# Kernel tuning notes

Hardware: AMD Instinct MI355X
Metric: run time of the kernel (lower is better)

## Reference

```python
import jax, jax.numpy as jnp
import numpy as np

N_T, N_C, N_M = 300000, 100000, 20000
D_IN, D, D_OUT = 390, 128, 64
H_PRE, H_POST = 256, 64


def _nrm(k, shape, scale=0.02):
    return jax.random.normal(k, shape, dtype=jnp.float32) * scale


def setup_inputs() -> dict:
    key = jax.random.key(0)
    ks = jax.random.split(key, 24)
    inp = {
        'input_features': jax.random.normal(ks[0], (N_T, D_IN), jnp.float32),
        'card_of_target': jax.random.randint(ks[1], (N_T,), 0, N_C, jnp.int32),
        'merchant_of_target': jax.random.randint(ks[2], (N_T,), 0, N_M, jnp.int32),
        # HeteroEmbedding tables for src types feeding 'target'
        'card_emb': _nrm(ks[3], (N_C, D)),
        'merch_emb': _nrm(ks[4], (N_M, D)),
        # target_preprocessing FFBlock (390 -> 256 -> 128, n_layers=2)
        'pre_Wi': _nrm(ks[5], (D_IN, H_PRE)), 'pre_bi': jnp.zeros((H_PRE,), jnp.float32),
        'pre_Wh': _nrm(ks[6], (H_PRE, H_PRE)), 'pre_bh': jnp.zeros((H_PRE,), jnp.float32),
        'pre_Wo': _nrm(ks[7], (H_PRE, D)), 'pre_bo': jnp.zeros((D,), jnp.float32),
        # conv1 / conv2: one GraphConv per etype; order:
        # 0=card->target, 1=merchant->target, 2=target->card, 3=target->merchant
        'conv1_W': _nrm(ks[8], (4, D, D)), 'conv1_b': jnp.zeros((4, D), jnp.float32),
        'conv2_W': _nrm(ks[9], (4, D, D)), 'conv2_b': jnp.zeros((4, D), jnp.float32),
        # conv3: dst=='target' -> D_OUT; dst!='target' -> 1
        'conv3_Wt': _nrm(ks[10], (2, D, D_OUT)), 'conv3_bt': jnp.zeros((2, D_OUT), jnp.float32),
        'conv3_Wo': _nrm(ks[11], (2, D, 1)), 'conv3_bo': jnp.zeros((2, 1), jnp.float32),
        # target_postprocessing FFBlock (64 -> 64 -> 1, n_layers=2)
        'post_Wi': _nrm(ks[12], (D_OUT, H_POST)), 'post_bi': jnp.zeros((H_POST,), jnp.float32),
        'post_Wh': _nrm(ks[13], (H_POST, H_POST)), 'post_bh': jnp.zeros((H_POST,), jnp.float32),
        'post_Wo': _nrm(ks[14], (H_POST, 1)), 'post_bo': jnp.zeros((1,), jnp.float32),
    }
    return inp


def _ff(x, Wi, bi, Wh, bh, Wo, bo, n_layers=2):
    h = jax.nn.relu(x @ Wi + bi)
    for _ in range(1, n_layers):
        h = jax.nn.relu(h @ Wh + bh)
    return h @ Wo + bo


def _deg(ids, n):
    # degree per node over edge endpoint list, clamped to >= 1 (DGL GraphConv)
    return jnp.maximum(jnp.zeros((n,), jnp.float32).at[ids].add(1.0), 1.0)


def _gconv(x_src, src, dst, n_dst, W, b, d_src, d_dst):
    # DGL GraphConv, norm='both': scale src by out_deg^-1/2, matmul,
    # sum messages onto dst, scale by in_deg^-1/2, add bias.
    h = (x_src * jax.lax.rsqrt(d_src)[:, None]) @ W          # [n_src, out]
    agg = jax.ops.segment_sum(h[src], dst, num_segments=n_dst)
    return agg * jax.lax.rsqrt(d_dst)[:, None] + b


def reference(input_features, card_of_target, merchant_of_target,
              card_emb, merch_emb,
              pre_Wi, pre_bi, pre_Wh, pre_bh, pre_Wo, pre_bo,
              conv1_W, conv1_b, conv2_W, conv2_b,
              conv3_Wt, conv3_bt, conv3_Wo, conv3_bo,
              post_Wi, post_bi, post_Wh, post_bh, post_Wo, post_bo):
    n_t, n_c, n_m = input_features.shape[0], card_emb.shape[0], merch_emb.shape[0]
    t_ids = jnp.arange(n_t, dtype=jnp.int32)
    d_c = _deg(card_of_target, n_c)      # card degree (in/out symmetric here)
    d_m = _deg(merchant_of_target, n_m)  # merchant degree
    d_t = _deg(t_ids, n_t)               # target degree (=1 per etype)

    tf = _ff(input_features, pre_Wi, pre_bi, pre_Wh, pre_bh, pre_Wo, pre_bo)

    # conv1 (HeteroGraphConv, aggregate='sum') + relu
    h1_t = (_gconv(card_emb, card_of_target, t_ids, n_t, conv1_W[0], conv1_b[0], d_c, d_t)
            + _gconv(merch_emb, merchant_of_target, t_ids, n_t, conv1_W[1], conv1_b[1], d_m, d_t))
    h1_c = _gconv(tf, t_ids, card_of_target, n_c, conv1_W[2], conv1_b[2], d_t, d_c)
    h1_m = _gconv(tf, t_ids, merchant_of_target, n_m, conv1_W[3], conv1_b[3], d_t, d_m)
    h1_t, h1_c, h1_m = jax.nn.relu(h1_t), jax.nn.relu(h1_c), jax.nn.relu(h1_m)

    # conv2 applied (conv_layers - 2) = 1 time
    h2_t, h2_c, h2_m = h1_t, h1_c, h1_m
    for _ in range(2, 3):
        n_t2 = (_gconv(h2_c, card_of_target, t_ids, n_t, conv2_W[0], conv2_b[0], d_c, d_t)
                + _gconv(h2_m, merchant_of_target, t_ids, n_t, conv2_W[1], conv2_b[1], d_m, d_t))
        n_c2 = _gconv(h2_t, t_ids, card_of_target, n_c, conv2_W[2], conv2_b[2], d_t, d_c)
        n_m2 = _gconv(h2_t, t_ids, merchant_of_target, n_m, conv2_W[3], conv2_b[3], d_t, d_m)
        h2_t, h2_c, h2_m = jax.nn.relu(n_t2), jax.nn.relu(n_c2), jax.nn.relu(n_m2)

    # conv3: D_OUT into target, 1 into non-target dsts; no relu
    h3_t = (_gconv(h2_c, card_of_target, t_ids, n_t, conv3_Wt[0], conv3_bt[0], d_c, d_t)
            + _gconv(h2_m, merchant_of_target, t_ids, n_t, conv3_Wt[1], conv3_bt[1], d_m, d_t))
    h3_c = _gconv(h2_t, t_ids, card_of_target, n_c, conv3_Wo[0], conv3_bo[0], d_t, d_c)
    h3_m = _gconv(h2_t, t_ids, merchant_of_target, n_m, conv3_Wo[1], conv3_bo[1], d_t, d_m)

    h3_t = _ff(h3_t, post_Wi, post_bi, post_Wh, post_bh, post_Wo, post_bo)
    return h3_t, h3_c, h3_m
```

## Files before the change

### kernel.cpp

```cpp
#include <hip/hip_runtime.h>


#define NT 300000
#define NC 100000
#define NM 20000
#define DIN 390
#define DD 128
#define DOUT 64
#define HPRE 256
#define HPOST 64

typedef _Float16 half8 __attribute__((ext_vector_type(8)));
typedef _Float16 half4v __attribute__((ext_vector_type(4)));
typedef float f32x16 __attribute__((ext_vector_type(16)));
typedef float f32x4 __attribute__((ext_vector_type(4)));

#define LO_SCALE 512.0f
#define LO_INV   (1.0f / 512.0f)

__device__ __forceinline__ void split2(float x, _Float16& h, _Float16& l) {
    _Float16 hh = (_Float16)x;
    h = hh;
    l = (_Float16)((x - (float)hh) * LO_SCALE);
}

__device__ __forceinline__ void gload16(const _Float16* g, _Float16* l) {
    __builtin_amdgcn_global_load_lds(
        (const __attribute__((address_space(1))) void*)g,
        (__attribute__((address_space(3))) void*)l, 16, 0, 0);
}

template<int TN>
__global__ __launch_bounds__(512, 4) void gemm_ps(
    const _Float16* __restrict__ Agh, const _Float16* __restrict__ Agl,
    const _Float16* __restrict__ Bgh, const _Float16* __restrict__ Bgl,
    const float* __restrict__ bias, const float* __restrict__ rowscale,
    _Float16* __restrict__ Ch, _Float16* __restrict__ Cl,
    float* __restrict__ C32,
    int M, int Kpad, int N, int relu)
{
    constexpr int BM = 128;
    constexpr int BN = 64 * TN;
    constexpr int OFF_AH = 0;
    constexpr int OFF_AL = 4096;
    constexpr int OFF_BH = 8192;
    constexpr int OFF_BL = 8192 + BN * 32;
    constexpr int BUFH   = 8192 + 2 * BN * 32;
    constexpr int NLD    = (TN == 2) ? 4 : 3;
    __shared__ __align__(16) _Float16 smem[2 * BUFH];

    const int tid  = (int)threadIdx.x;
    const int lane = tid & 63;
    const int wave = tid >> 6;
    const int wm0  = (wave & 3) * 32;
    const int wn0  = (wave >> 2) * 32 * TN;

    const int nbn  = N / BN;
    const int bm   = ((int)blockIdx.x / nbn) * BM;
    const int bn   = ((int)blockIdx.x % nbn) * BN;

    const int srow = lane >> 2;
    const int xc8  = (((lane & 3) ^ (srow & 3)) << 3);
    const size_t a_off = (size_t)(bm + wave * 16 + srow) * Kpad + xc8;
    size_t b_off;
    if constexpr (TN == 2) {
        b_off = (size_t)(bn + wave * 16 + srow) * Kpad + xc8;
    } else {
        b_off = (size_t)(bn + (wave & 3) * 16 + srow) * Kpad + xc8;
    }

    auto stage = [&](int b, int k0) {
        _Float16* sb = &smem[b * BUFH];
        gload16(Agh + a_off + k0, sb + OFF_AH + wave * 512);
        gload16(Agl + a_off + k0, sb + OFF_AL + wave * 512);
        if constexpr (TN == 2) {
            gload16(Bgh + b_off + k0, sb + OFF_BH + wave * 512);
            gload16(Bgl + b_off + k0, sb + OFF_BL + wave * 512);
        } else {
            gload16((wave < 4 ? Bgh : Bgl) + b_off + k0,
                    sb + (wave < 4 ? OFF_BH : OFF_BL) + (wave & 3) * 512);
        }
    };

    f32x16 zz;
    #pragma unroll
    for (int i = 0; i < 16; ++i) zz[i] = 0.f;
    f32x16 acc_hh[TN], acc_x[TN];
    #pragma unroll
    for (int t2 = 0; t2 < TN; ++t2) { acc_hh[t2] = zz; acc_x[t2] = zz; }

    const int mlr = lane & 31;
    const int hi5 = lane >> 5;
    const int xr  = mlr & 3;

    const int NS = Kpad >> 5;
    stage(0, 0);

    for (int t = 0; t < NS; ++t) {
        if (t + 1 < NS) {
            stage((t + 1) & 1, (t + 1) << 5);
            asm volatile("s_waitcnt vmcnt(%0)" :: "n"(NLD) : "memory");
        } else {
            asm volatile("s_waitcnt vmcnt(0)" ::: "memory");
        }
        __builtin_amdgcn_s_barrier();
        __builtin_amdgcn_sched_barrier(0);

        const _Float16* sb = &smem[(t & 1) * BUFH];
        #pragma unroll
        for (int ks = 0; ks < 2; ++ks) {
            const int xo = (((ks * 2 + hi5) ^ xr) << 3);
            const half8 fah = *(const half8*)&sb[OFF_AH + (wm0 + mlr) * 32 + xo];
            const half8 fal = *(const half8*)&sb[OFF_AL + (wm0 + mlr) * 32 + xo];
            half8 fbh[TN], fbl[TN];
            #pragma unroll
            for (int t2 = 0; t2 < TN; ++t2) {
                const int nn = wn0 + t2 * 32 + mlr;
                fbh[t2] = *(const half8*)&sb[OFF_BH + nn * 32 + xo];
                fbl[t2] = *(const half8*)&sb[OFF_BL + nn * 32 + xo];
            }
            #pragma unroll
            for (int t2 = 0; t2 < TN; ++t2) {
                acc_hh[t2] = __builtin_amdgcn_mfma_f32_32x32x16_f16(
                    fah, fbh[t2], acc_hh[t2], 0, 0, 0);
                acc_x[t2] = __builtin_amdgcn_mfma_f32_32x32x16_f16(
                    fah, fbl[t2], acc_x[t2], 0, 0, 0);
                acc_x[t2] = __builtin_amdgcn_mfma_f32_32x32x16_f16(
                    fal, fbh[t2], acc_x[t2], 0, 0, 0);
            }
        }
        __builtin_amdgcn_sched_barrier(0);
        __builtin_amdgcn_s_barrier();
    }

    const int r0 = 4 * hi5;
    #pragma unroll
    for (int t2 = 0; t2 < TN; ++t2) {
        const int gcol = bn + wn0 + t2 * 32 + mlr;
        const float bc = (bias != nullptr) ? bias[gcol] : 0.f;
        #pragma unroll
        for (int r = 0; r < 16; ++r) {
            const int grow = bm + wm0 + (r & 3) + r0 + 8 * (r >> 2);
            if (grow < M) {
                float v = acc_hh[t2][r] + acc_x[t2][r] * LO_INV;
                if (rowscale != nullptr) v *= rowscale[grow];
                v += bc;
                if (relu) v = fmaxf(v, 0.f);
                if (C32 != nullptr) {
                    C32[(size_t)grow * N + gcol] = v;
                } else {
                    _Float16 hh, ll;
                    split2(v, hh, ll);
                    Ch[(size_t)grow * N + gcol] = hh;
                    Cl[(size_t)grow * N + gcol] = ll;
                }
            }
        }
    }
}

template<int TM, int TN, int WGM, int WGN>
__global__ __launch_bounds__(256, 3) void gemm_mfma(
    const float* __restrict__ A, const _Float16* __restrict__ Wh,
    const _Float16* __restrict__ Wl, const float* __restrict__ bias,
    const float* __restrict__ rowscale,
    float* __restrict__ C32, _Float16* __restrict__ Ch, _Float16* __restrict__ Cl,
    int M, int K, int N, int Kpad, int relu)
{
    constexpr int BM = 32 * TM * WGM;
    constexpr int BN = 32 * TN * WGN;
    constexpr int RS = 40;
    __shared__ __align__(16) _Float16 Ah[BM * RS];
    __shared__ __align__(16) _Float16 Al[BM * RS];
    __shared__ __align__(16) _Float16 Bh[BN * RS];
    __shared__ __align__(16) _Float16 Bl[BN * RS];

    const int tid  = (int)threadIdx.x;
    const int lane = tid & 63;
    const int wave = tid >> 6;
    const int wm0 = (wave % WGM) * 32 * TM;
    const int wn0 = (wave / WGM) * 32 * TN;

    const int nbn = N / BN;
    const int tile = (int)blockIdx.x;
    const int bm = (tile / nbn) * BM;
    const int bn = (tile % nbn) * BN;

    f32x16 zz;
    #pragma unroll
    for (int i = 0; i < 16; ++i) zz[i] = 0.f;
    f32x16 acc_hh[TM][TN], acc_x[TM][TN];
    #pragma unroll
    for (int tm = 0; tm < TM; ++tm)
        #pragma unroll
        for (int tn = 0; tn < TN; ++tn) { acc_hh[tm][tn] = zz; acc_x[tm][tn] = zz; }

    constexpr int TPR  = 256 / BM;
    constexpr int KPT  = 32 / TPR;
    constexpr int FQ   = KPT / 4;
    const int sar = tid / TPR;
    const int sak = (tid % TPR) * KPT;
    const int agrow = bm + sar;
    const float* Aptr = A + (size_t)agrow * K;

    constexpr int TPRB = 256 / BN;
    constexpr int KPTB = 32 / TPRB;
    constexpr int NB   = KPTB / 8;
    const int sbr = tid / TPRB;
    const int sbk = (tid % TPRB) * KPTB;
    const _Float16* Bhp = Wh + (size_t)(bn + sbr) * Kpad + sbk;
    const _Float16* Blp = Wl + (size_t)(bn + sbr) * Kpad + sbk;

    const int ml  = lane & 31;
    const int klo = (lane >> 5) * 8;

    f32x4 areg[FQ];
    half8 bhreg[NB], blreg[NB];

    auto loadA = [&](int k0) {
        #pragma unroll
        for (int q = 0; q < FQ; ++q) {
            const int kb = k0 + sak + q * 4;
            f32x4 f = {0.f, 0.f, 0.f, 0.f};
            if (agrow < M) {
                if (kb + 3 < K) {
                    f = *(const f32x4*)(Aptr + kb);
                } else {
                    if (kb + 0 < K) f[0] = Aptr[kb + 0];
                    if (kb + 1 < K) f[1] = Aptr[kb + 1];
                    if (kb + 2 < K) f[2] = Aptr[kb + 2];
                    if (kb + 3 < K) f[3] = Aptr[kb + 3];
                }
            }
            areg[q] = f;
        }
    };
    auto loadB = [&](int k0) {
        #pragma unroll
        for (int j = 0; j < NB; ++j) {
            bhreg[j] = *(const half8*)(Bhp + k0 + j * 8);
            blreg[j] = *(const half8*)(Blp + k0 + j * 8);
        }
    };

    loadA(0);
    loadB(0);

    for (int k0 = 0; k0 < K; k0 += 32) {
        #pragma unroll
        for (int c = 0; c < FQ / 2; ++c) {
            half8 h, l;
            #pragma unroll
            for (int q = 0; q < 2; ++q) {
                #pragma unroll
                for (int j = 0; j < 4; ++j) {
                    _Float16 th, tl;
                    split2(areg[2 * c + q][j], th, tl);
                    h[q * 4 + j] = th;
                    l[q * 4 + j] = tl;
                }
            }
            *(half8*)&Ah[sar * RS + sak + c * 8] = h;
            *(half8*)&Al[sar * RS + sak + c * 8] = l;
        }
        #pragma unroll
        for (int j = 0; j < NB; ++j) {
            *(half8*)&Bh[sbr * RS + sbk + j * 8] = bhreg[j];
            *(half8*)&Bl[sbr * RS + sbk + j * 8] = blreg[j];
        }
        __syncthreads();

        if (k0 + 32 < K) { loadA(k0 + 32); loadB(k0 + 32); }

        #pragma unroll
        for (int ks = 0; ks < 2; ++ks) {
            const int kk = ks * 16 + klo;
            half8 fah[TM], fal[TM], fbh[TN], fbl[TN];
            #pragma unroll
            for (int t = 0; t < TM; ++t) {
                const int m = wm0 + t * 32 + ml;
                fah[t] = *(const half8*)&Ah[m * RS + kk];
                fal[t] = *(const half8*)&Al[m * RS + kk];
            }
            #pragma unroll
            for (int t = 0; t < TN; ++t) {
                const int n = wn0 + t * 32 + ml;
                fbh[t] = *(const half8*)&Bh[n * RS + kk];
                fbl[t] = *(const half8*)&Bl[n * RS + kk];
            }
            #pragma unroll
            for (int tm = 0; tm < TM; ++tm)
                #pragma unroll
                for (int tn = 0; tn < TN; ++tn) {
                    acc_hh[tm][tn] = __builtin_amdgcn_mfma_f32_32x32x16_f16(
                        fah[tm], fbh[tn], acc_hh[tm][tn], 0, 0, 0);
                    acc_x[tm][tn] = __builtin_amdgcn_mfma_f32_32x32x16_f16(
                        fah[tm], fbl[tn], acc_x[tm][tn], 0, 0, 0);
                    acc_x[tm][tn] = __builtin_amdgcn_mfma_f32_32x32x16_f16(
                        fal[tm], fbh[tn], acc_x[tm][tn], 0, 0, 0);
                }
        }
        __syncthreads();
    }

    const int r0 = 4 * (lane >> 5);
    #pragma unroll
    for (int tm = 0; tm < TM; ++tm) {
        #pragma unroll
        for (int tn = 0; tn < TN; ++tn) {
            const int gcol = bn + wn0 + tn * 32 + ml;
            const float bc = (bias != nullptr) ? bias[gcol] : 0.f;
            #pragma unroll
            for (int r = 0; r < 16; ++r) {
                const int grow = bm + wm0 + tm * 32 + (r & 3) + r0 + 8 * (r >> 2);
                if (grow < M) {
                    float v = acc_hh[tm][tn][r] + acc_x[tm][tn][r] * LO_INV;
                    if (rowscale != nullptr) v *= rowscale[grow];
                    v += bc;
                    if (relu) v = fmaxf(v, 0.f);
                    if (C32 != nullptr) {
                        C32[(size_t)grow * N + gcol] = v;
                    } else {
                        _Float16 hh, ll;
                        split2(v, hh, ll);
                        Ch[(size_t)grow * N + gcol] = hh;
                        Cl[(size_t)grow * N + gcol] = ll;
                    }
                }
            }
        }
    }
}

__global__ void split_w(const float* __restrict__ W, _Float16* __restrict__ hiT,
                        _Float16* __restrict__ loT, int K, int N, int Kpad, int nmat)
{
    int idx = blockIdx.x * blockDim.x + threadIdx.x;
    int total = nmat * N * Kpad;
    if (idx >= total) return;
    int e = idx / (N * Kpad);
    int rem = idx - e * (N * Kpad);
    int n = rem / Kpad;
    int k = rem - n * Kpad;
    float v = (k < K) ? W[((size_t)e * K + k) * N + n] : 0.f;
    _Float16 h = (_Float16)v;
    hiT[idx] = h;
    loT[idx] = (_Float16)((v - (float)h) * LO_SCALE);
}

__global__ void split_a(const float* __restrict__ X, _Float16* __restrict__ xh,
                        _Float16* __restrict__ xl, int M, int Mpad, int K)
{
    int idx = blockIdx.x * blockDim.x + threadIdx.x;
    int per = K >> 3;
    int total = Mpad * per;
    if (idx >= total) return;
    int row = idx / per;
    int k = (idx - row * per) << 3;
    half8 h, l;
    if (row < M) {
        #pragma unroll
        for (int j = 0; j < 8; ++j) {
            _Float16 th, tl;
            split2(X[(size_t)row * K + k + j], th, tl);
            h[j] = th; l[j] = tl;
        }
    } else {
        #pragma unroll
        for (int j = 0; j < 8; ++j) { h[j] = (_Float16)0.f; l[j] = (_Float16)0.f; }
    }
    *(half8*)&xh[(size_t)row * K + k] = h;
    *(half8*)&xl[(size_t)row * K + k] = l;
}

__global__ void count_kernel(const int* __restrict__ card, const int* __restrict__ merch,
                             int* cnt_c, int* cnt_m, int n)
{
    int t = blockIdx.x * blockDim.x + threadIdx.x;
    if (t >= n) return;
    atomicAdd(&cnt_c[card[t]], 1);
    atomicAdd(&cnt_m[merch[t]], 1);
}

__global__ void rsqrt_kernel(const int* __restrict__ cnt, float* __restrict__ rs, int n)
{
    int i = blockIdx.x * blockDim.x + threadIdx.x;
    if (i >= n) return;
    int c = cnt[i];
    if (c < 1) c = 1;
    rs[i] = 1.0f / sqrtf((float)c);
}

__global__ __launch_bounds__(1024) void scan_excl(const int* __restrict__ cnt,
                                                  int* __restrict__ off, int n)
{
    __shared__ int wsum[16];
    const int tid = (int)threadIdx.x;
    const int lane = tid & 63, wid = tid >> 6;
    int carry = 0;
    for (int base = 0; base < n; base += 1024) {
        int i = base + tid;
        int v = (i < n) ? cnt[i] : 0;
        int x = v;
        #pragma unroll
        for (int d = 1; d < 64; d <<= 1) {
            int y = __shfl_up(x, d);
            if (lane >= d) x += y;
        }
        if (lane == 63) wsum[wid] = x;
        __syncthreads();
        int wpre = 0, tot = 0;
        #pragma unroll
        for (int w = 0; w < 16; ++w) {
            int s = wsum[w];
            if (w < wid) wpre += s;
            tot += s;
        }
        if (i < n) off[i] = carry + wpre + (x - v);
        carry += tot;
        __syncthreads();
    }
    if (tid == 0) off[n] = carry;
}

__global__ void fill_sorted(const int* __restrict__ ids, const int* __restrict__ off,
                            int* cur, int* __restrict__ srt, int n)
{
    int t = blockIdx.x * blockDim.x + threadIdx.x;
    if (t >= n) return;
    int c = ids[t];
    int p = atomicAdd(&cur[c], 1);
    srt[off[c] + p] = t;
}

__global__ void gather2_kernel(const float* __restrict__ hc, const float* __restrict__ hm,
                               const int* __restrict__ card, const int* __restrict__ merch,
                               const float* __restrict__ b0, const float* __restrict__ b1,
                               float* __restrict__ out32, _Float16* __restrict__ oh,
                               _Float16* __restrict__ ol, int n, int dim, int relu)
{
    int idx = blockIdx.x * blockDim.x + threadIdx.x;
    int per = dim >> 2;
    int t = idx / per;
    if (t >= n) return;
    int d4 = (idx % per) << 2;
    int c = card[t], m = merch[t];
    float4 a = *(const float4*)(hc + (size_t)c * dim + d4);
    float4 b = *(const float4*)(hm + (size_t)m * dim + d4);
    float4 v0 = *(const float4*)(b0 + d4);
    float4 v1 = *(const float4*)(b1 + d4);
    float4 r;
    r.x = a.x + b.x + v0.x + v1.x;
    r.y = a.y + b.y + v0.y + v1.y;
    r.z = a.z + b.z + v0.z + v1.z;
    r.w = a.w + b.w + v0.w + v1.w;
    if (relu) {
        r.x = fmaxf(r.x, 0.f); r.y = fmaxf(r.y, 0.f);
        r.z = fmaxf(r.z, 0.f); r.w = fmaxf(r.w, 0.f);
    }
    if (out32 != nullptr) {
        *(float4*)(out32 + (size_t)t * dim + d4) = r;
    } else {
        half4v h, l;
        _Float16 th, tl;
        split2(r.x, th, tl); h[0] = th; l[0] = tl;
        split2(r.y, th, tl); h[1] = th; l[1] = tl;
        split2(r.z, th, tl); h[2] = th; l[2] = tl;
        split2(r.w, th, tl); h[3] = th; l[3] = tl;
        *(half4v*)&oh[(size_t)t * dim + d4] = h;
        *(half4v*)&ol[(size_t)t * dim + d4] = l;
    }
}

__global__ __launch_bounds__(256) void agg_csr_kernel(
    const float* __restrict__ proj, const int* __restrict__ off,
    const int* __restrict__ srt, const float* __restrict__ rs,
    const float* __restrict__ bias, _Float16* __restrict__ oh,
    _Float16* __restrict__ ol, int n, int relu)
{
    int node = blockIdx.x * 2 + ((int)threadIdx.x >> 7);
    int d = (int)threadIdx.x & 127;
    if (node >= n) return;
    int s = off[node], e = off[node + 1];
    float acc = 0.f;
    for (int i = s; i < e; ++i) {
        int t = srt[i];
        acc += proj[(size_t)t * 128 + d];
    }
    float v = acc * rs[node] + bias[d];
    if (relu) v = fmaxf(v, 0.f);
    _Float16 hh, ll;
    split2(v, hh, ll);
    oh[(size_t)node * 128 + d] = hh;
    ol[(size_t)node * 128 + d] = ll;
}

__global__ __launch_bounds__(256) void dot2_kernel(
    const float* __restrict__ h, const float* __restrict__ w0,
    const float* __restrict__ w1, float* __restrict__ s2, int n)
{
    int row = blockIdx.x * 4 + ((int)threadIdx.x >> 6);
    int l = (int)threadIdx.x & 63;
    if (row >= n) return;
    const float* x = h + (size_t)row * 128;
    float x0 = x[l], x1 = x[l + 64];
    float p0 = x0 * w0[l] + x1 * w0[l + 64];
    float p1 = x0 * w1[l] + x1 * w1[l + 64];
    #pragma unroll
    for (int o = 32; o > 0; o >>= 1) {
        p0 += __shfl_down(p0, o);
        p1 += __shfl_down(p1, o);
    }
    if (l == 0) { s2[(size_t)row * 2] = p0; s2[(size_t)row * 2 + 1] = p1; }
}

__global__ void agg_scalar_kernel(const float* __restrict__ s2, int which,
                                  const int* __restrict__ off, const int* __restrict__ srt,
                                  const float* __restrict__ rs, const float* __restrict__ bias,
                                  float* __restrict__ out, int n)
{
    int node = blockIdx.x * blockDim.x + threadIdx.x;
    if (node >= n) return;
    float acc = 0.f;
    int e = off[node + 1];
    for (int i = off[node]; i < e; ++i) acc += s2[(size_t)srt[i] * 2 + which];
    out[node] = acc * rs[node] + bias[0];
}

__global__ __launch_bounds__(256) void dot1_kernel(
    const float* __restrict__ h, const float* __restrict__ w,
    const float* __restrict__ b, float* __restrict__ out, int n)
{
    int row = blockIdx.x * 4 + ((int)threadIdx.x >> 6);
    int l = (int)threadIdx.x & 63;
    if (row >= n) return;
    float p = h[(size_t)row * 64 + l] * w[l];
    #pragma unroll
    for (int o = 32; o > 0; o >>= 1) p += __shfl_down(p, o);
    if (l == 0) out[row] = p + b[0];
}

static inline void gemm_ps_launch(const _Float16* Ah, const _Float16* Al,
    const _Float16* Bh, const _Float16* Bl, const float* bias, const float* rs,
    _Float16* Ch, _Float16* Cl, float* C32,
    int M, int Kpad, int N, int relu, hipStream_t s)
{
    const int nbm = (M + 127) / 128;
    if (N % 128 == 0) {
        gemm_ps<2><<<dim3(nbm * (N / 128)), 512, 0, s>>>(
            Ah, Al, Bh, Bl, bias, rs, Ch, Cl, C32, M, Kpad, N, relu);
    } else {
        gemm_ps<1><<<dim3(nbm), 512, 0, s>>>(
            Ah, Al, Bh, Bl, bias, rs, Ch, Cl, C32, M, Kpad, N, relu);
    }
}

#define PAD128(x) ((((x) + 127) / 128) * 128)

extern "C" void kernel_launch(void* const* d_in, const int* in_sizes, int n_in,
                              void* d_out, int out_size, void* d_ws, size_t ws_size,
                              hipStream_t stream)
{
    const float* x_in      = (const float*)d_in[0];
    const int*   card      = (const int*)d_in[1];
    const int*   merch     = (const int*)d_in[2];
    const float* card_emb  = (const float*)d_in[3];
    const float* merch_emb = (const float*)d_in[4];
    const float* pre_Wi = (const float*)d_in[5];
    const float* pre_bi = (const float*)d_in[6];
    const float* pre_Wh = (const float*)d_in[7];
    const float* pre_bh = (const float*)d_in[8];
    const float* pre_Wo = (const float*)d_in[9];
    const float* pre_bo = (const float*)d_in[10];
    const float* conv1_W = (const float*)d_in[11];
    const float* conv1_b = (const float*)d_in[12];
    const float* conv2_W = (const float*)d_in[13];
    const float* conv2_b = (const float*)d_in[14];
    const float* conv3_Wt = (const float*)d_in[15];
    const float* conv3_bt = (const float*)d_in[16];
    const float* conv3_Wo = (const float*)d_in[17];
    const float* conv3_bo = (const float*)d_in[18];
    const float* post_Wi = (const float*)d_in[19];
    const float* post_bi = (const float*)d_in[20];
    const float* post_Wh = (const float*)d_in[21];
    const float* post_bh = (const float*)d_in[22];
    const float* post_Wo = (const float*)d_in[23];
    const float* post_bo = (const float*)d_in[24];

    float* out = (float*)d_out;

    const int MTP = PAD128(NT);
    const int MCP = PAD128(NC);
    const int MMP = PAD128(NM);

    char* ws = (char*)d_ws;
    size_t off = 0;
    auto alloc = [&](size_t bytes) -> char* {
        char* p = ws + off;
        off += (bytes + 255) & ~(size_t)255;
        return p;
    };
    int* cnt_c = (int*)alloc((size_t)NC * 4);
    int* cnt_m = (int*)alloc((size_t)NM * 4);
    int* cur_c = (int*)alloc((size_t)NC * 4);
    int* cur_m = (int*)alloc((size_t)NM * 4);
    size_t zero_bytes = (size_t)((char*)(cur_m + NM) - (char*)cnt_c);
    int* off_c = (int*)alloc((size_t)(NC + 1) * 4);
    int* off_m = (int*)alloc((size_t)(NM + 1) * 4);
    int* srt_c = (int*)alloc((size_t)NT * 4);
    int* srt_m = (int*)alloc((size_t)NT * 4);
    float* rs_c = (float*)alloc((size_t)NC * 4);
    float* rs_m = (float*)alloc((size_t)NM * 4);

    const int KP_WI = 416;
    _Float16* wi_h  = (_Float16*)alloc((size_t)HPRE * KP_WI * 2);
    _Float16* wi_l  = (_Float16*)alloc((size_t)HPRE * KP_WI * 2);
    _Float16* wh_h  = (_Float16*)alloc((size_t)HPRE * HPRE * 2);
    _Float16* wh_l  = (_Float16*)alloc((size_t)HPRE * HPRE * 2);
    _Float16* wo_h  = (_Float16*)alloc((size_t)DD * HPRE * 2);
    _Float16* wo_l  = (_Float16*)alloc((size_t)DD * HPRE * 2);
    _Float16* c1_h  = (_Float16*)alloc((size_t)4 * DD * DD * 2);
    _Float16* c1_l  = (_Float16*)alloc((size_t)4 * DD * DD * 2);
    _Float16* c2_h  = (_Float16*)alloc((size_t)4 * DD * DD * 2);
    _Float16* c2_l  = (_Float16*)alloc((size_t)4 * DD * DD * 2);
    _Float16* c3_h  = (_Float16*)alloc((size_t)2 * DOUT * DD * 2);
    _Float16* c3_l  = (_Float16*)alloc((size_t)2 * DOUT * DD * 2);
    _Float16* pi_h  = (_Float16*)alloc((size_t)HPOST * DOUT * 2);
    _Float16* pi_l  = (_Float16*)alloc((size_t)HPOST * DOUT * 2);
    _Float16* ph_h  = (_Float16*)alloc((size_t)HPOST * HPOST * 2);
    _Float16* ph_l  = (_Float16*)alloc((size_t)HPOST * HPOST * 2);

    _Float16* ce_h   = (_Float16*)alloc((size_t)MCP * DD * 2);
    _Float16* ce_l   = (_Float16*)alloc((size_t)MCP * DD * 2);
    _Float16* me_h   = (_Float16*)alloc((size_t)MMP * DD * 2);
    _Float16* me_l   = (_Float16*)alloc((size_t)MMP * DD * 2);
    _Float16* bufA_h = (_Float16*)alloc((size_t)MTP * HPRE * 2);
    _Float16* bufA_l = (_Float16*)alloc((size_t)MTP * HPRE * 2);
    _Float16* bufB_h = (_Float16*)alloc((size_t)MTP * HPRE * 2);
    _Float16* bufB_l = (_Float16*)alloc((size_t)MTP * HPRE * 2);
    _Float16* tf_h   = (_Float16*)alloc((size_t)MTP * DD * 2);
    _Float16* tf_l   = (_Float16*)alloc((size_t)MTP * DD * 2);
    _Float16* h1t_h  = (_Float16*)alloc((size_t)MTP * DD * 2);
    _Float16* h1t_l  = (_Float16*)alloc((size_t)MTP * DD * 2);
    _Float16* h1c_h  = (_Float16*)alloc((size_t)MCP * DD * 2);
    _Float16* h1c_l  = (_Float16*)alloc((size_t)MCP * DD * 2);
    _Float16* h1m_h  = (_Float16*)alloc((size_t)MMP * DD * 2);
    _Float16* h1m_l  = (_Float16*)alloc((size_t)MMP * DD * 2);
    _Float16* h2c_h  = (_Float16*)alloc((size_t)MCP * DD * 2);
    _Float16* h2c_l  = (_Float16*)alloc((size_t)MCP * DD * 2);
    _Float16* h2m_h  = (_Float16*)alloc((size_t)MMP * DD * 2);
    _Float16* h2m_l  = (_Float16*)alloc((size_t)MMP * DD * 2);
    _Float16* h3_h   = (_Float16*)alloc((size_t)MTP * DOUT * 2);
    _Float16* h3_l   = (_Float16*)alloc((size_t)MTP * DOUT * 2);
    _Float16* p1_h   = (_Float16*)alloc((size_t)MTP * DOUT * 2);
    _Float16* p1_l   = (_Float16*)alloc((size_t)MTP * DOUT * 2);

    float* proj = (float*)alloc((size_t)MTP * DD * 4);
    float* h2_t = (float*)alloc((size_t)MTP * DD * 4);
    float* hc_p = (float*)alloc((size_t)MCP * DD * 4);
    float* hm_p = (float*)alloc((size_t)MMP * DD * 4);
    float* p2   = (float*)alloc((size_t)MTP * DOUT * 4);
    float* s2   = (float*)alloc((size_t)NT * 2 * 4);
    (void)ws_size; (void)in_sizes; (void)n_in; (void)out_size;

    hipMemsetAsync(cnt_c, 0, zero_bytes, stream);
    count_kernel<<<(NT + 255) / 256, 256, 0, stream>>>(card, merch, cnt_c, cnt_m, NT);
    rsqrt_kernel<<<(NC + 255) / 256, 256, 0, stream>>>(cnt_c, rs_c, NC);
    rsqrt_kernel<<<(NM + 255) / 256, 256, 0, stream>>>(cnt_m, rs_m, NM);
    scan_excl<<<1, 1024, 0, stream>>>(cnt_c, off_c, NC);
    scan_excl<<<1, 1024, 0, stream>>>(cnt_m, off_m, NM);
    fill_sorted<<<(NT + 255) / 256, 256, 0, stream>>>(card, off_c, cur_c, srt_c, NT);
    fill_sorted<<<(NT + 255) / 256, 256, 0, stream>>>(merch, off_m, cur_m, srt_m, NT);

    auto splitw = [&](const float* W, _Float16* h, _Float16* l, int K, int N, int Kpad, int nmat) {
        int total = nmat * N * Kpad;
        split_w<<<(total + 255) / 256, 256, 0, stream>>>(W, h, l, K, N, Kpad, nmat);
    };
    splitw(pre_Wi,   wi_h, wi_l, DIN,  HPRE,  KP_WI, 1);
    splitw(pre_Wh,   wh_h, wh_l, HPRE, HPRE,  HPRE,  1);
    splitw(pre_Wo,   wo_h, wo_l, HPRE, DD,    HPRE,  1);
    splitw(conv1_W,  c1_h, c1_l, DD,   DD,    DD,    4);
    splitw(conv2_W,  c2_h, c2_l, DD,   DD,    DD,    4);
    splitw(conv3_Wt, c3_h, c3_l, DD,   DOUT,  DD,    2);
    splitw(post_Wi,  pi_h, pi_l, DOUT, HPOST, DOUT,  1);
    splitw(post_Wh,  ph_h, ph_l, HPOST,HPOST, HPOST, 1);

    split_a<<<((MCP * (DD / 8)) + 255) / 256, 256, 0, stream>>>(card_emb, ce_h, ce_l, NC, MCP, DD);
    split_a<<<((MMP * (DD / 8)) + 255) / 256, 256, 0, stream>>>(merch_emb, me_h, me_l, NM, MMP, DD);

    const int WP  = DD * DD;
    const int WP3 = DOUT * DD;

    {
        const int nbm = (NT + 63) / 64;
        gemm_mfma<1, 2, 2, 2><<<dim3(nbm * 2), 256, 0, stream>>>(
            x_in, wi_h, wi_l, pre_bi, nullptr, nullptr, bufA_h, bufA_l,
            NT, DIN, HPRE, KP_WI, 1);
    }
    gemm_ps_launch(bufA_h, bufA_l, wh_h, wh_l, pre_bh, nullptr,
                   bufB_h, bufB_l, nullptr, NT, HPRE, HPRE, 1, stream);
    gemm_ps_launch(bufB_h, bufB_l, wo_h, wo_l, pre_bo, nullptr,
                   tf_h, tf_l, nullptr, NT, HPRE, DD, 0, stream);

    gemm_ps_launch(ce_h, ce_l, c1_h + 0 * WP, c1_l + 0 * WP, nullptr, rs_c,
                   nullptr, nullptr, hc_p, NC, DD, DD, 0, stream);
    gemm_ps_launch(me_h, me_l, c1_h + 1 * WP, c1_l + 1 * WP, nullptr, rs_m,
                   nullptr, nullptr, hm_p, NM, DD, DD, 0, stream);
    gather2_kernel<<<(NT * (DD / 4) + 255) / 256, 256, 0, stream>>>(
        hc_p, hm_p, card, merch, conv1_b, conv1_b + DD,
        nullptr, h1t_h, h1t_l, NT, DD, 1);
    gemm_ps_launch(tf_h, tf_l, c1_h + 2 * WP, c1_l + 2 * WP, nullptr, nullptr,
                   nullptr, nullptr, proj, NT, DD, DD, 0, stream);
    agg_csr_kernel<<<(NC + 1) / 2, 256, 0, stream>>>(proj, off_c, srt_c, rs_c,
                                                     conv1_b + 2 * DD, h1c_h, h1c_l, NC, 1);
    gemm_ps_launch(tf_h, tf_l, c1_h + 3 * WP, c1_l + 3 * WP, nullptr, nullptr,
                   nullptr, nullptr, proj, NT, DD, DD, 0, stream);
    agg_csr_kernel<<<(NM + 1) / 2, 256, 0, stream>>>(proj, off_m, srt_m, rs_m,
                                                     conv1_b + 3 * DD, h1m_h, h1m_l, NM, 1);

    gemm_ps_launch(h1c_h, h1c_l, c2_h + 0 * WP, c2_l + 0 * WP, nullptr, rs_c,
                   nullptr, nullptr, hc_p, NC, DD, DD, 0, stream);
    gemm_ps_launch(h1m_h, h1m_l, c2_h + 1 * WP, c2_l + 1 * WP, nullptr, rs_m,
                   nullptr, nullptr, hm_p, NM, DD, DD, 0, stream);
    gather2_kernel<<<(NT * (DD / 4) + 255) / 256, 256, 0, stream>>>(
        hc_p, hm_p, card, merch, conv2_b, conv2_b + DD,
        h2_t, nullptr, nullptr, NT, DD, 1);
    gemm_ps_launch(h1t_h, h1t_l, c2_h + 2 * WP, c2_l + 2 * WP, nullptr, nullptr,
                   nullptr, nullptr, proj, NT, DD, DD, 0, stream);
    agg_csr_kernel<<<(NC + 1) / 2, 256, 0, stream>>>(proj, off_c, srt_c, rs_c,
                                                     conv2_b + 2 * DD, h2c_h, h2c_l, NC, 1);
    gemm_ps_launch(h1t_h, h1t_l, c2_h + 3 * WP, c2_l + 3 * WP, nullptr, nullptr,
                   nullptr, nullptr, proj, NT, DD, DD, 0, stream);
    agg_csr_kernel<<<(NM + 1) / 2, 256, 0, stream>>>(proj, off_m, srt_m, rs_m,
                                                     conv2_b + 3 * DD, h2m_h, h2m_l, NM, 1);

    gemm_ps_launch(h2c_h, h2c_l, c3_h + 0 * WP3, c3_l + 0 * WP3, nullptr, rs_c,
                   nullptr, nullptr, hc_p, NC, DD, DOUT, 0, stream);
    gemm_ps_launch(h2m_h, h2m_l, c3_h + 1 * WP3, c3_l + 1 * WP3, nullptr, rs_m,
                   nullptr, nullptr, hm_p, NM, DD, DOUT, 0, stream);
    gather2_kernel<<<(NT * (DOUT / 4) + 255) / 256, 256, 0, stream>>>(
        hc_p, hm_p, card, merch, conv3_bt, conv3_bt + DOUT,
        nullptr, h3_h, h3_l, NT, DOUT, 0);
    dot2_kernel<<<(NT + 3) / 4, 256, 0, stream>>>(h2_t, conv3_Wo, conv3_Wo + DD, s2, NT);
    agg_scalar_kernel<<<(NC + 255) / 256, 256, 0, stream>>>(s2, 0, off_c, srt_c, rs_c,
                                                            conv3_bo + 0, out + NT, NC);
    agg_scalar_kernel<<<(NM + 255) / 256, 256, 0, stream>>>(s2, 1, off_m, srt_m, rs_m,
                                                            conv3_bo + 1, out + NT + NC, NM);

    gemm_ps_launch(h3_h, h3_l, pi_h, pi_l, post_bi, nullptr,
                   p1_h, p1_l, nullptr, NT, DOUT, HPOST, 1, stream);
    gemm_ps_launch(p1_h, p1_l, ph_h, ph_l, post_bh, nullptr,
                   nullptr, nullptr, p2, NT, HPOST, HPOST, 1, stream);
    dot1_kernel<<<(NT + 3) / 4, 256, 0, stream>>>(p2, post_Wo, post_bo, out, NT);
}
```

Before: 2.761 ms.

## Fuse post-FF chain, merge target projections, deepen GEMM prefetch pipelines

Several unrelated changes land together. The conv3 gather, both post-processing GEMMs and the final dot product are fused into one post_ff kernel that keeps intermediates in LDS. The two target-side projections per conv layer become one GEMM with N=256, read by both CSR aggregations through a stride and offset. The main GEMM gets a triple-buffered A stage with a new LDS swizzle, and the fp32-input GEMM gets register double-buffering. This removes launches and HBM round trips, at the cost of more LDS and registers and some risk of lower occupancy.

After: 2.796 ms. About the same (+1.3%).

```diff
diff --git a/kernel.cpp b/kernel.cpp
--- a/kernel.cpp
+++ b/kernel.cpp
@@ -41,13 +41,10 @@
 {
     constexpr int BM = 128;
     constexpr int BN = 64 * TN;
-    constexpr int OFF_AH = 0;
-    constexpr int OFF_AL = 4096;
-    constexpr int OFF_BH = 8192;
-    constexpr int OFF_BL = 8192 + BN * 32;
-    constexpr int BUFH   = 8192 + 2 * BN * 32;
-    constexpr int NLD    = (TN == 2) ? 4 : 3;
-    __shared__ __align__(16) _Float16 smem[2 * BUFH];
+    constexpr int BHALF = BN * 32;
+    constexpr int BUFB  = 2 * BHALF;
+    constexpr int OFF_B = 24576;
+    __shared__ __align__(16) _Float16 smem[OFF_B + 2 * BUFB];
 
     const int tid  = (int)threadIdx.x;
     const int lane = tid & 63;
@@ -60,7 +57,7 @@
     const int bn   = ((int)blockIdx.x % nbn) * BN;
 
     const int srow = lane >> 2;
-    const int xc8  = (((lane & 3) ^ (srow & 3)) << 3);
+    const int xc8  = (((lane & 3) ^ ((srow >> 1) & 3)) << 3);
     const size_t a_off = (size_t)(bm + wave * 16 + srow) * Kpad + xc8;
     size_t b_off;
     if constexpr (TN == 2) {
@@ -69,16 +66,19 @@
         b_off = (size_t)(bn + (wave & 3) * 16 + srow) * Kpad + xc8;
     }
 
-    auto stage = [&](int b, int k0) {
-        _Float16* sb = &smem[b * BUFH];
-        gload16(Agh + a_off + k0, sb + OFF_AH + wave * 512);
-        gload16(Agl + a_off + k0, sb + OFF_AL + wave * 512);
+    auto stageA = [&](int ab, int k0) {
+        _Float16* base = &smem[ab * 8192];
+        gload16(Agh + a_off + k0, base + wave * 512);
+        gload16(Agl + a_off + k0, base + 4096 + wave * 512);
+    };
+    auto stageB = [&](int bb, int k0) {
+        _Float16* base = &smem[OFF_B + bb * BUFB];
         if constexpr (TN == 2) {
-            gload16(Bgh + b_off + k0, sb + OFF_BH + wave * 512);
-            gload16(Bgl + b_off + k0, sb + OFF_BL + wave * 512);
+            gload16(Bgh + b_off + k0, base + wave * 512);
+            gload16(Bgl + b_off + k0, base + BHALF + wave * 512);
         } else {
             gload16((wave < 4 ? Bgh : Bgl) + b_off + k0,
-                    sb + (wave < 4 ? OFF_BH : OFF_BL) + (wave & 3) * 512);
+                    base + (wave < 4 ? 0 : BHALF) + (wave & 3) * 512);
         }
     };
 
@@ -91,33 +91,43 @@
 
     const int mlr = lane & 31;
     const int hi5 = lane >> 5;
-    const int xr  = mlr & 3;
+    const int xr  = (mlr >> 1) & 3;
 
     const int NS = Kpad >> 5;
-    stage(0, 0);
+
+    stageB(0, 0);
+    stageA(0, 0);
+    if (NS > 1) stageA(1, 32);
+
+    int ca = 0, cn = 2;
 
     for (int t = 0; t < NS; ++t) {
-        if (t + 1 < NS) {
-            stage((t + 1) & 1, (t + 1) << 5);
-            asm volatile("s_waitcnt vmcnt(%0)" :: "n"(NLD) : "memory");
+        if (t + 1 < NS) stageB((t + 1) & 1, (t + 1) << 5);
+        if (t + 2 < NS) stageA(cn, (t + 2) << 5);
+
+        if (t + 2 < NS) {
+            asm volatile("s_waitcnt vmcnt(%0)" :: "n"(TN == 2 ? 6 : 5) : "memory");
+        } else if (t + 1 < NS) {
+            asm volatile("s_waitcnt vmcnt(%0)" :: "n"(TN == 2 ? 4 : 3) : "memory");
         } else {
             asm volatile("s_waitcnt vmcnt(0)" ::: "memory");
         }
         __builtin_amdgcn_s_barrier();
         __builtin_amdgcn_sched_barrier(0);
 
-        const _Float16* sb = &smem[(t & 1) * BUFH];
+        const _Float16* sa = &smem[ca * 8192];
+        const _Float16* sb = &smem[OFF_B + (t & 1) * BUFB];
         #pragma unroll
         for (int ks = 0; ks < 2; ++ks) {
             const int xo = (((ks * 2 + hi5) ^ xr) << 3);
-            const half8 fah = *(const half8*)&sb[OFF_AH + (wm0 + mlr) * 32 + xo];
-            const half8 fal = *(const half8*)&sb[OFF_AL + (wm0 + mlr) * 32 + xo];
+            const half8 fah = *(const half8*)&sa[(wm0 + mlr) * 32 + xo];
+            const half8 fal = *(const half8*)&sa[4096 + (wm0 + mlr) * 32 + xo];
             half8 fbh[TN], fbl[TN];
             #pragma unroll
             for (int t2 = 0; t2 < TN; ++t2) {
                 const int nn = wn0 + t2 * 32 + mlr;
-                fbh[t2] = *(const half8*)&sb[OFF_BH + nn * 32 + xo];
-                fbl[t2] = *(const half8*)&sb[OFF_BL + nn * 32 + xo];
+                fbh[t2] = *(const half8*)&sb[nn * 32 + xo];
+                fbl[t2] = *(const half8*)&sb[BHALF + nn * 32 + xo];
             }
             #pragma unroll
             for (int t2 = 0; t2 < TN; ++t2) {
@@ -131,6 +141,9 @@
         }
         __builtin_amdgcn_sched_barrier(0);
         __builtin_amdgcn_s_barrier();
+
+        ca = (ca == 2) ? 0 : ca + 1;
+        cn = (cn == 2) ? 0 : cn + 1;
     }
 
     const int r0 = 4 * hi5;
@@ -214,10 +227,10 @@
     const int ml  = lane & 31;
     const int klo = (lane >> 5) * 8;
 
-    f32x4 areg[FQ];
-    half8 bhreg[NB], blreg[NB];
-
-    auto loadA = [&](int k0) {
+    f32x4 areg0[FQ], areg1[FQ];
+    half8 bh0[NB], bl0[NB], bh1[NB], bl1[NB];
+
+    auto loadA = [&](f32x4 (&ar)[FQ], int k0) {
         #pragma unroll
         for (int q = 0; q < FQ; ++q) {
             const int kb = k0 + sak + q * 4;
@@ -232,21 +245,22 @@
                     if (kb + 3 < K) f[3] = Aptr[kb + 3];
                 }
             }
-            areg[q] = f;
+            ar[q] = f;
         }
     };
-    auto loadB = [&](int k0) {
+    auto loadB = [&](half8 (&bh)[NB], half8 (&bl)[NB], int k0) {
         #pragma unroll
         for (int j = 0; j < NB; ++j) {
-            bhreg[j] = *(const half8*)(Bhp + k0 + j * 8);
-            blreg[j] = *(const half8*)(Blp + k0 + j * 8);
+            bh[j] = *(const half8*)(Bhp + k0 + j * 8);
+            bl[j] = *(const half8*)(Blp + k0 + j * 8);
         }
     };
 
-    loadA(0);
-    loadB(0);
-
-    for (int k0 = 0; k0 < K; k0 += 32) {
+    loadA(areg0, 0);
+    loadB(bh0, bl0, 0);
+    if (32 < K) { loadA(areg1, 32); loadB(bh1, bl1, 32); }
+
+    auto step = [&](f32x4 (&ar)[FQ], half8 (&bh)[NB], half8 (&bl)[NB], int k0) {
         #pragma unroll
         for (int c = 0; c < FQ / 2; ++c) {
             half8 h, l;
@@ -255,7 +269,7 @@
                 #pragma unroll
                 for (int j = 0; j < 4; ++j) {
                     _Float16 th, tl;
-                    split2(areg[2 * c + q][j], th, tl);
+                    split2(ar[2 * c + q][j], th, tl);
                     h[q * 4 + j] = th;
                     l[q * 4 + j] = tl;
                 }
@@ -265,12 +279,12 @@
         }
         #pragma unroll
         for (int j = 0; j < NB; ++j) {
-            *(half8*)&Bh[sbr * RS + sbk + j * 8] = bhreg[j];
-            *(half8*)&Bl[sbr * RS + sbk + j * 8] = blreg[j];
+            *(half8*)&Bh[sbr * RS + sbk + j * 8] = bh[j];
+            *(half8*)&Bl[sbr * RS + sbk + j * 8] = bl[j];
         }
         __syncthreads();
 
-        if (k0 + 32 < K) { loadA(k0 + 32); loadB(k0 + 32); }
+        if (k0 + 64 < K) { loadA(ar, k0 + 64); loadB(bh, bl, k0 + 64); }
 
         #pragma unroll
         for (int ks = 0; ks < 2; ++ks) {
@@ -301,6 +315,11 @@
                 }
         }
         __syncthreads();
+    };
+
+    for (int k0 = 0; k0 < K; k0 += 64) {
+        step(areg0, bh0, bl0, k0);
+        if (k0 + 32 < K) step(areg1, bh1, bl1, k0 + 32);
     }
 
     const int r0 = 4 * (lane >> 5);
@@ -332,6 +351,152 @@
     }
 }
 
+__global__ __launch_bounds__(512, 2) void post_ff(
+    const float* __restrict__ hc, const float* __restrict__ hm,
+    const int* __restrict__ card, const int* __restrict__ merch,
+    const float* __restrict__ bt0, const float* __restrict__ bt1,
+    const _Float16* __restrict__ wih, const _Float16* __restrict__ wil,
+    const float* __restrict__ bi,
+    const _Float16* __restrict__ whh, const _Float16* __restrict__ whl,
+    const float* __restrict__ bh,
+    const float* __restrict__ wo, const float* __restrict__ bo,
+    float* __restrict__ out, int n)
+{
+    constexpr int SR = 72;
+    constexpr int OFF_AH = 0;
+    constexpr int OFF_AL = 9216;
+    constexpr int OFF_HH = 18432;
+    constexpr int OFF_HL = 27648;
+    constexpr int OFF_W1H = 36864;
+    constexpr int OFF_W1L = 41472;
+    constexpr int OFF_W2H = 46080;
+    constexpr int OFF_W2L = 50688;
+    __shared__ __align__(16) _Float16 S[55296];
+    float* sh2 = (float*)&S[OFF_AH];
+
+    const int tid  = (int)threadIdx.x;
+    const int lane = tid & 63;
+    const int wave = tid >> 6;
+    const int bm   = (int)blockIdx.x * 128;
+
+    {
+        const int wn = (tid & 255) >> 2;
+        const int c0 = (tid & 3) * 16;
+        const _Float16* gh = (tid < 256) ? wih : whh;
+        const _Float16* gl = (tid < 256) ? wil : whl;
+        const int oh = (tid < 256) ? OFF_W1H : OFF_W2H;
+        const int ol = (tid < 256) ? OFF_W1L : OFF_W2L;
+        *(half8*)&S[oh + wn * SR + c0]     = *(const half8*)(gh + wn * 64 + c0);
+        *(half8*)&S[oh + wn * SR + c0 + 8] = *(const half8*)(gh + wn * 64 + c0 + 8);
+        *(half8*)&S[ol + wn * SR + c0]     = *(const half8*)(gl + wn * 64 + c0);
+        *(half8*)&S[ol + wn * SR + c0 + 8] = *(const half8*)(gl + wn * 64 + c0 + 8);
+    }
+    {
+        const int r  = tid >> 2;
+        const int c0 = (tid & 3) << 4;
+        const int t  = bm + r;
+        const bool ok = (t < n);
+        const int ci = ok ? card[t] : 0;
+        const int mi = ok ? merch[t] : 0;
+        #pragma unroll
+        for (int q = 0; q < 4; ++q) {
+            const int c = c0 + q * 4;
+            float4 a = make_float4(0.f, 0.f, 0.f, 0.f);
+            if (ok) {
+                float4 va = *(const float4*)(hc + (size_t)ci * 64 + c);
+                float4 vb = *(const float4*)(hm + (size_t)mi * 64 + c);
+                float4 b0 = *(const float4*)(bt0 + c);
+                float4 b1 = *(const float4*)(bt1 + c);
+                a.x = va.x + vb.x + b0.x + b1.x;
+                a.y = va.y + vb.y + b0.y + b1.y;
+                a.z = va.z + vb.z + b0.z + b1.z;
+                a.w = va.w + vb.w + b0.w + b1.w;
+            }
+            half4v h, l;
+            _Float16 th, tl;
+            split2(a.x, th, tl); h[0] = th; l[0] = tl;
+            split2(a.y, th, tl); h[1] = th; l[1] = tl;
+            split2(a.z, th, tl); h[2] = th; l[2] = tl;
+            split2(a.w, th, tl); h[3] = th; l[3] = tl;
+            *(half4v*)&S[OFF_AH + r * SR + c] = h;
+            *(half4v*)&S[OFF_AL + r * SR + c] = l;
+        }
+    }
+    __syncthreads();
+
+    const int mlr = lane & 31;
+    const int hi5 = lane >> 5;
+    const int wm = (wave & 3) * 32;
+    const int wn = (wave >> 2) * 32;
+    const int r0 = 4 * hi5;
+
+    f32x16 zz;
+    #pragma unroll
+    for (int i = 0; i < 16; ++i) zz[i] = 0.f;
+
+    {
+        f32x16 acc = zz, accx = zz;
+        #pragma unroll
+        for (int ks = 0; ks < 4; ++ks) {
+            const int kk = ks * 16 + hi5 * 8;
+            const half8 fah = *(const half8*)&S[OFF_AH + (wm + mlr) * SR + kk];
+            const half8 fal = *(const half8*)&S[OFF_AL + (wm + mlr) * SR + kk];
+            const half8 fbh = *(const half8*)&S[OFF_W1H + (wn + mlr) * SR + kk];
+            const half8 fbl = *(const half8*)&S[OFF_W1L + (wn + mlr) * SR + kk];
+            acc  = __builtin_amdgcn_mfma_f32_32x32x16_f16(fah, fbh, acc, 0, 0, 0);
+            accx = __builtin_amdgcn_mfma_f32_32x32x16_f16(fah, fbl, accx, 0, 0, 0);
+            accx = __builtin_amdgcn_mfma_f32_32x32x16_f16(fal, fbh, accx, 0, 0, 0);
+        }
+        const float bc = bi[wn + mlr];
+        __syncthreads();
+        #pragma unroll
+        for (int r = 0; r < 16; ++r) {
+            const int row = wm + (r & 3) + r0 + 8 * (r >> 2);
+            float v = acc[r] + accx[r] * LO_INV + bc;
+            v = fmaxf(v, 0.f);
+            _Float16 hh, ll;
+            split2(v, hh, ll);
+            S[OFF_HH + row * SR + wn + mlr] = hh;
+            S[OFF_HL + row * SR + wn + mlr] = ll;
+        }
+    }
+    __syncthreads();
+
+    {
+        f32x16 acc = zz, accx = zz;
+        #pragma unroll
+        for (int ks = 0; ks < 4; ++ks) {
+            const int kk = ks * 16 + hi5 * 8;
+            const half8 fah = *(const half8*)&S[OFF_HH + (wm + mlr) * SR + kk];
+            const half8 fal = *(const half8*)&S[OFF_HL + (wm + mlr) * SR + kk];
+            const half8 fbh = *(const half8*)&S[OFF_W2H + (wn + mlr) * SR + kk];
+            const half8 fbl = *(const half8*)&S[OFF_W2L + (wn + mlr) * SR + kk];
+            acc  = __builtin_amdgcn_mfma_f32_32x32x16_f16(fah, fbh, acc, 0, 0, 0);
+            accx = __builtin_amdgcn_mfma_f32_32x32x16_f16(fah, fbl, accx, 0, 0, 0);
+            accx = __builtin_amdgcn_mfma_f32_32x32x16_f16(fal, fbh, accx, 0, 0, 0);
+        }
+        const float bc = bh[wn + mlr];
+        __syncthreads();
+        #pragma unroll
+        for (int r = 0; r < 16; ++r) {
+            const int row = wm + (r & 3) + r0 + 8 * (r >> 2);
+            float v = acc[r] + accx[r] * LO_INV + bc;
+            sh2[row * 68 + wn + mlr] = fmaxf(v, 0.f);
+        }
+    }
+    __syncthreads();
+
+    if (tid < 128) {
+        const int t = bm + tid;
+        if (t < n) {
+            float s = bo[0];
+            #pragma unroll 8
+            for (int c = 0; c < 64; ++c) s += sh2[tid * 68 + c] * wo[c];
+            out[t] = s;
+        }
+    }
+}
+
 __global__ void split_w(const float* __restrict__ W, _Float16* __restrict__ hiT,
                         _Float16* __restrict__ loT, int K, int N, int Kpad, int nmat)
 {
@@ -473,10 +638,10 @@
 }
 
 __global__ __launch_bounds__(256) void agg_csr_kernel(
-    const float* __restrict__ proj, const int* __restrict__ off,
-    const int* __restrict__ srt, const float* __restrict__ rs,
-    const float* __restrict__ bias, _Float16* __restrict__ oh,
-    _Float16* __restrict__ ol, int n, int relu)
+    const float* __restrict__ proj, int ldp, int doff,
+    const int* __restrict__ off, const int* __restrict__ srt,
+    const float* __restrict__ rs, const float* __restrict__ bias,
+    _Float16* __restrict__ oh, _Float16* __restrict__ ol, int n, int relu)
 {
     int node = blockIdx.x * 2 + ((int)threadIdx.x >> 7);
     int d = (int)threadIdx.x & 127;
@@ -485,7 +650,7 @@
     float acc = 0.f;
     for (int i = s; i < e; ++i) {
         int t = srt[i];
-        acc += proj[(size_t)t * 128 + d];
+        acc += proj[(size_t)t * ldp + doff + d];
     }
     float v = acc * rs[node] + bias[d];
     if (relu) v = fmaxf(v, 0.f);
@@ -525,19 +690,6 @@
     int e = off[node + 1];
     for (int i = off[node]; i < e; ++i) acc += s2[(size_t)srt[i] * 2 + which];
     out[node] = acc * rs[node] + bias[0];
-}
-
-__global__ __launch_bounds__(256) void dot1_kernel(
-    const float* __restrict__ h, const float* __restrict__ w,
-    const float* __restrict__ b, float* __restrict__ out, int n)
-{
-    int row = blockIdx.x * 4 + ((int)threadIdx.x >> 6);
-    int l = (int)threadIdx.x & 63;
-    if (row >= n) return;
-    float p = h[(size_t)row * 64 + l] * w[l];
-    #pragma unroll
-    for (int o = 32; o > 0; o >>= 1) p += __shfl_down(p, o);
-    if (l == 0) out[row] = p + b[0];
 }
 
 static inline void gemm_ps_launch(const _Float16* Ah, const _Float16* Al,
@@ -650,16 +802,11 @@
     _Float16* h2c_l  = (_Float16*)alloc((size_t)MCP * DD * 2);
     _Float16* h2m_h  = (_Float16*)alloc((size_t)MMP * DD * 2);
     _Float16* h2m_l  = (_Float16*)alloc((size_t)MMP * DD * 2);
-    _Float16* h3_h   = (_Float16*)alloc((size_t)MTP * DOUT * 2);
-    _Float16* h3_l   = (_Float16*)alloc((size_t)MTP * DOUT * 2);
-    _Float16* p1_h   = (_Float16*)alloc((size_t)MTP * DOUT * 2);
-    _Float16* p1_l   = (_Float16*)alloc((size_t)MTP * DOUT * 2);
-
-    float* proj = (float*)alloc((size_t)MTP * DD * 4);
+
+    float* proj = (float*)alloc((size_t)MTP * 256 * 4);
     float* h2_t = (float*)alloc((size_t)MTP * DD * 4);
     float* hc_p = (float*)alloc((size_t)MCP * DD * 4);
     float* hm_p = (float*)alloc((size_t)MMP * DD * 4);
-    float* p2   = (float*)alloc((size_t)MTP * DOUT * 4);
     float* s2   = (float*)alloc((size_t)NT * 2 * 4);
     (void)ws_size; (void)in_sizes; (void)n_in; (void)out_size;
 
@@ -710,12 +857,10 @@
         hc_p, hm_p, card, merch, conv1_b, conv1_b + DD,
         nullptr, h1t_h, h1t_l, NT, DD, 1);
     gemm_ps_launch(tf_h, tf_l, c1_h + 2 * WP, c1_l + 2 * WP, nullptr, nullptr,
-                   nullptr, nullptr, proj, NT, DD, DD, 0, stream);
-    agg_csr_kernel<<<(NC + 1) / 2, 256, 0, stream>>>(proj, off_c, srt_c, rs_c,
+                   nullptr, nullptr, proj, NT, DD, 256, 0, stream);
+    agg_csr_kernel<<<(NC + 1) / 2, 256, 0, stream>>>(proj, 256, 0, off_c, srt_c, rs_c,
                                                      conv1_b + 2 * DD, h1c_h, h1c_l, NC, 1);
-    gemm_ps_launch(tf_h, tf_l, c1_h + 3 * WP, c1_l + 3 * WP, nullptr, nullptr,
-                   nullptr, nullptr, proj, NT, DD, DD, 0, stream);
-    agg_csr_kernel<<<(NM + 1) / 2, 256, 0, stream>>>(proj, off_m, srt_m, rs_m,
+    agg_csr_kernel<<<(NM + 1) / 2, 256, 0, stream>>>(proj, 256, 128, off_m, srt_m, rs_m,
                                                      conv1_b + 3 * DD, h1m_h, h1m_l, NM, 1);
 
     gemm_ps_launch(h1c_h, h1c_l, c2_h + 0 * WP, c2_l + 0 * WP, nullptr, rs_c,
@@ -726,30 +871,23 @@
         hc_p, hm_p, card, merch, conv2_b, conv2_b + DD,
         h2_t, nullptr, nullptr, NT, DD, 1);
     gemm_ps_launch(h1t_h, h1t_l, c2_h + 2 * WP, c2_l + 2 * WP, nullptr, nullptr,
-                   nullptr, nullptr, proj, NT, DD, DD, 0, stream);
-    agg_csr_kernel<<<(NC + 1) / 2, 256, 0, stream>>>(proj, off_c, srt_c, rs_c,
+                   nullptr, nullptr, proj, NT, DD, 256, 0, stream);
+    agg_csr_kernel<<<(NC + 1) / 2, 256, 0, stream>>>(proj, 256, 0, off_c, srt_c, rs_c,
                                                      conv2_b + 2 * DD, h2c_h, h2c_l, NC, 1);
-    gemm_ps_launch(h1t_h, h1t_l, c2_h + 3 * WP, c2_l + 3 * WP, nullptr, nullptr,
-                   nullptr, nullptr, proj, NT, DD, DD, 0, stream);
-    agg_csr_kernel<<<(NM + 1) / 2, 256, 0, stream>>>(proj, off_m, srt_m, rs_m,
+    agg_csr_kernel<<<(NM + 1) / 2, 256, 0, stream>>>(proj, 256, 128, off_m, srt_m, rs_m,
                                                      conv2_b + 3 * DD, h2m_h, h2m_l, NM, 1);
 
     gemm_ps_launch(h2c_h, h2c_l, c3_h + 0 * WP3, c3_l + 0 * WP3, nullptr, rs_c,
                    nullptr, nullptr, hc_p, NC, DD, DOUT, 0, stream);
     gemm_ps_launch(h2m_h, h2m_l, c3_h + 1 * WP3, c3_l + 1 * WP3, nullptr, rs_m,
                    nullptr, nullptr, hm_p, NM, DD, DOUT, 0, stream);
-    gather2_kernel<<<(NT * (DOUT / 4) + 255) / 256, 256, 0, stream>>>(
-        hc_p, hm_p, card, merch, conv3_bt, conv3_bt + DOUT,
-        nullptr, h3_h, h3_l, NT, DOUT, 0);
     dot2_kernel<<<(NT + 3) / 4, 256, 0, stream>>>(h2_t, conv3_Wo, conv3_Wo + DD, s2, NT);
     agg_scalar_kernel<<<(NC + 255) / 256, 256, 0, stream>>>(s2, 0, off_c, srt_c, rs_c,
                                                             conv3_bo + 0, out + NT, NC);
     agg_scalar_kernel<<<(NM + 255) / 256, 256, 0, stream>>>(s2, 1, off_m, srt_m, rs_m,
                                                             conv3_bo + 1, out + NT + NC, NM);
 
-    gemm_ps_launch(h3_h, h3_l, pi_h, pi_l, post_bi, nullptr,
-                   p1_h, p1_l, nullptr, NT, DOUT, HPOST, 1, stream);
-    gemm_ps_launch(p1_h, p1_l, ph_h, ph_l, post_bh, nullptr,
-                   nullptr, nullptr, p2, NT, HPOST, HPOST, 1, stream);
-    dot1_kernel<<<(NT + 3) / 4, 256, 0, stream>>>(p2, post_Wo, post_bo, out, NT);
-}
+    post_ff<<<dim3((NT + 127) / 128), 512, 0, stream>>>(
+        hc_p, hm_p, card, merch, conv3_bt, conv3_bt + DOUT,
+        pi_h, pi_l, post_bi, ph_h, ph_l, post_bh, post_Wo, post_bo, out, NT);
+}
```
